# Optimization experiments

Measured on AMD Instinct MI355X. Metric: run time of the kernel, lower is better.

The kernel has to match this reference:

```python
import jax, jax.numpy as jnp
import numpy as np

B, L, H = 2, 2048, 2048
DI, N, DTR, K = 4096, 16, 128, 4  # intermediate, state, dt_rank, conv kernel


def setup_inputs() -> dict:
    key = jax.random.key(0)
    ks = jax.random.split(key, 8)
    x = jax.random.normal(ks[0], (B, L, H), jnp.float32)
    in_proj_w = jax.random.normal(ks[1], (2 * DI, H), jnp.float32) * 0.02
    conv1d_w = jax.random.normal(ks[2], (DI, 1, K), jnp.float32) * 0.1
    conv1d_b = jnp.zeros((DI,), jnp.float32)
    x_proj_w = jax.random.normal(ks[3], (DTR + 2 * N, DI), jnp.float32) * 0.02
    bound = DTR ** -0.5
    dt_proj_w = jax.random.uniform(ks[4], (DI, DTR), jnp.float32, -bound, bound)
    # faithful dt bias init: inverse-softplus of dt ~ Uniform-log[0.001, 0.1]
    dt = jnp.exp(jax.random.uniform(ks[5], (DI,), jnp.float32)
                 * (np.log(0.1) - np.log(0.001)) + np.log(0.001))
    dt = jnp.clip(dt, 1e-4)
    dt_proj_b = dt + jnp.log(-jnp.expm1(-dt))
    A_log = jnp.log(jnp.broadcast_to(jnp.arange(1, N + 1, dtype=jnp.float32), (DI, N)))
    D = jnp.ones((DI,), jnp.float32)
    out_proj_w = jax.random.normal(ks[6], (H, DI), jnp.float32) * 0.02
    return dict(x=x, in_proj_w=in_proj_w, conv1d_w=conv1d_w, conv1d_b=conv1d_b,
                x_proj_w=x_proj_w, dt_proj_w=dt_proj_w, dt_proj_b=dt_proj_b,
                A_log=A_log, D=D, out_proj_w=out_proj_w)


def _mamba_forward(x, in_proj_w, conv1d_w, conv1d_b, x_proj_w,
                   dt_proj_w, dt_proj_b, A_log, D, out_proj_w):
    # in_proj -> split into ssm input and gate (res)
    x_and_res = jnp.einsum('blh,eh->ble', x, in_proj_w)          # [B,L,2*DI]
    xi, res = jnp.split(x_and_res, 2, axis=-1)                    # [B,L,DI] each

    # depthwise causal conv1d (kernel K, left-pad K-1, truncated to L)
    xc = jnp.transpose(xi, (0, 2, 1))                             # [B,DI,L]
    xc = jax.lax.conv_general_dilated(
        xc, conv1d_w, window_strides=(1,), padding=((K - 1, 0),),
        dimension_numbers=('NCH', 'OIH', 'NCH'), feature_group_count=DI)
    xc = xc + conv1d_b[None, :, None]
    u = jax.nn.silu(jnp.transpose(xc, (0, 2, 1)))                 # [B,L,DI]

    # selective SSM parameters
    A = -jnp.exp(A_log.astype(jnp.float32))                       # [DI,N]
    x_dbl = jnp.einsum('bld,ed->ble', u, x_proj_w)                # [B,L,DTR+2N]
    dlt, Bm, Cm = jnp.split(x_dbl, [DTR, DTR + N], axis=-1)
    delta = jax.nn.softplus(jnp.einsum('blr,dr->bld', dlt, dt_proj_w) + dt_proj_b)

    # selective scan over time; carry h: [B,DI,N]
    def step(h, inp):
        d_t, B_t, C_t, u_t = inp                                  # [B,DI],[B,N],[B,N],[B,DI]
        dA = jnp.exp(d_t[:, :, None] * A)                         # [B,DI,N]
        h = dA * h + d_t[:, :, None] * B_t[:, None, :] * u_t[:, :, None]
        y_t = jnp.einsum('bdn,bn->bd', h, C_t)
        return h, y_t

    xs = (jnp.transpose(delta, (1, 0, 2)), jnp.transpose(Bm, (1, 0, 2)),
          jnp.transpose(Cm, (1, 0, 2)), jnp.transpose(u, (1, 0, 2)))
    h0 = jnp.zeros((x.shape[0], DI, N), jnp.float32)
    _, ys = jax.lax.scan(step, h0, xs)                            # ys: [L,B,DI]
    y = jnp.transpose(ys, (1, 0, 2)) + u * D.astype(jnp.float32)  # skip via D

    y = y * jax.nn.silu(res)                                      # gate
    return jnp.einsum('bld,hd->blh', y, out_proj_w)               # [B,L,H]


def reference(x, in_proj_w, conv1d_w, conv1d_b, x_proj_w,
              dt_proj_w, dt_proj_b, A_log, D, out_proj_w):
    return _mamba_forward(x, in_proj_w, conv1d_w, conv1d_b, x_proj_w,
                          dt_proj_w, dt_proj_b, A_log, D, out_proj_w)
```

## Files before the change

kernel.cpp:

```cpp
#include <hip/hip_runtime.h>
#include <hip/hip_bf16.h>
#include <stdint.h>

#define DEV static __device__ __forceinline__

typedef __attribute__((ext_vector_type(8))) short short8;
typedef __attribute__((ext_vector_type(4))) float f32x4;
typedef __attribute__((address_space(3))) void lds_void;
typedef __attribute__((address_space(1))) void glb_void;

constexpr int CB = 2, CL = 2048, CH = 2048, CDI = 4096, CN = 16, CDTR = 128;
constexpr int BLR = CB * CL;
constexpr int NC = 32, LC = 64;
constexpr int KSL = 8;

DEV ushort f2b(float f) {
  union { float f; uint32_t u; } v; v.f = f;
  uint32_t u = v.u;
  return (ushort)((u + 0x7fffu + ((u >> 16) & 1u)) >> 16);
}
DEV float b2f(ushort b) {
  union { uint32_t u; float f; } v; v.u = ((uint32_t)b) << 16;
  return v.f;
}
DEV void gload16(const ushort* g, ushort* l) {
  __builtin_amdgcn_global_load_lds((const glb_void*)g, (lds_void*)l, 16, 0, 0);
}
DEV f32x4 mfma16(short8 a, short8 b, f32x4 c) {
  return __builtin_amdgcn_mfma_f32_16x16x32_bf16(a, b, c, 0, 0, 0);
}

__global__ void cast_kernel(const float* __restrict__ in, ushort* __restrict__ out, int n4) {
  int i = blockIdx.x * blockDim.x + threadIdx.x;
  if (i >= n4) return;
  float4 v = *(const float4*)(in + (size_t)i * 4);
  *(ushort4*)(out + (size_t)i * 4) = make_ushort4(f2b(v.x), f2b(v.y), f2b(v.z), f2b(v.w));
}

__global__ void cast_pad_xproj_kernel(const float* __restrict__ in, ushort* __restrict__ out) {
  int i = blockIdx.x * blockDim.x + threadIdx.x;
  if (i >= (256 * 4096 / 4)) return;
  int idx = i * 4;
  int r = idx >> 12;
  ushort4 o;
  if (r < 160) {
    float4 v = *(const float4*)(in + idx);
    o = make_ushort4(f2b(v.x), f2b(v.y), f2b(v.z), f2b(v.w));
  } else {
    o = make_ushort4(0, 0, 0, 0);
  }
  *(ushort4*)(out + idx) = o;
}

__global__ void conv_silu_kernel(const ushort* __restrict__ xr, const float* __restrict__ w,
                                 const float* __restrict__ bias, ushort* __restrict__ u) {
  int t = blockIdx.x * blockDim.x + threadIdx.x;
  if (t >= BLR * CDI / 8) return;
  const int d8 = (t & (CDI / 8 - 1)) << 3;
  const int bl = t >> 9;
  const int l = bl & (CL - 1);
  float a[8];
  {
    float4 b0 = *(const float4*)(bias + d8);
    float4 b1 = *(const float4*)(bias + d8 + 4);
    a[0] = b0.x; a[1] = b0.y; a[2] = b0.z; a[3] = b0.w;
    a[4] = b1.x; a[5] = b1.y; a[6] = b1.z; a[7] = b1.w;
  }
  float wk[8][4];
#pragma unroll
  for (int j = 0; j < 8; ++j) {
    float4 wj = *(const float4*)(w + (size_t)(d8 + j) * 4);
    wk[j][0] = wj.x; wk[j][1] = wj.y; wk[j][2] = wj.z; wk[j][3] = wj.w;
  }
#pragma unroll
  for (int k = 0; k < 4; ++k) {
    if (l - 3 + k >= 0) {
      short8 xv = *(const short8*)(xr + (size_t)(bl - 3 + k) * 8192 + d8);
#pragma unroll
      for (int j = 0; j < 8; ++j)
        a[j] = fmaf(wk[j][k], b2f((ushort)xv[j]), a[j]);
    }
  }
  short8 o;
#pragma unroll
  for (int j = 0; j < 8; ++j) {
    float s = a[j] / (1.f + __expf(-a[j]));
    o[j] = (short)f2b(s);
  }
  *(short8*)(u + (size_t)bl * 4096 + d8) = o;
}

template<int EPI>
__global__ __launch_bounds__(256, 4)
void gemm_bt_kernel(const ushort* __restrict__ A, const ushort* __restrict__ Bw,
                    void* __restrict__ Cp, const float* __restrict__ bias,
                    int M, int N, int K) {
  __shared__ ushort sA[128 * 32];
  __shared__ ushort sB[128 * 32];
  const int tid = threadIdx.x;
  const int bm = blockIdx.x, bn = blockIdx.y;
  const int w = tid >> 6, l = tid & 63;
  const int wr = w >> 1, wc = w & 1;
  const int q = l >> 4, r = l & 15;

  f32x4 acc[4][4] = {};

  const ushort* Ab = A + (size_t)bm * 128 * K;
  const ushort* Bb = Bw + (size_t)bn * 128 * K;
  const int nk = K >> 5;
  for (int kt = 0; kt < nk; ++kt) {
    const int k0 = kt << 5;
#pragma unroll
    for (int i = 0; i < 2; ++i) {
      const int chunk = i * 256 + tid;
      const int row = chunk >> 2;
      const int cofs = (chunk & 3) << 3;
      gload16(Ab + (size_t)row * K + k0 + cofs, sA + chunk * 8);
      gload16(Bb + (size_t)row * K + k0 + cofs, sB + chunk * 8);
    }
    __syncthreads();
    short8 af[4], bfg[4];
#pragma unroll
    for (int i = 0; i < 4; ++i) {
      af[i]  = *(const short8*)(sA + (wr * 64 + i * 16 + r) * 32 + q * 8);
      bfg[i] = *(const short8*)(sB + (wc * 64 + i * 16 + r) * 32 + q * 8);
    }
#pragma unroll
    for (int i = 0; i < 4; ++i)
#pragma unroll
      for (int j = 0; j < 4; ++j)
        acc[i][j] = mfma16(af[i], bfg[j], acc[i][j]);
    __syncthreads();
  }

  const int m0 = bm * 128 + wr * 64;
  const int n0 = bn * 128 + wc * 64;
#pragma unroll
  for (int i = 0; i < 4; ++i) {
#pragma unroll
    for (int j = 0; j < 4; ++j) {
#pragma unroll
      for (int v = 0; v < 4; ++v) {
        const int grow = m0 + i * 16 + q * 4 + v;
        const int gcol = n0 + j * 16 + r;
        const float val = acc[i][j][v];
        if (EPI == 0) {
          ((ushort*)Cp)[(size_t)grow * N + gcol] = f2b(val);
        } else if (EPI == 1) {
          ((float*)Cp)[(size_t)grow * N + gcol] = val;
        } else {
          float xv = val + bias[gcol];
          float sp = xv > 20.f ? xv : log1pf(__expf(xv));
          ((ushort*)Cp)[(size_t)grow * N + gcol] = f2b(sp);
        }
      }
    }
  }
}

template<int EPI>
__global__ __launch_bounds__(512, 1)
void gemm256p_kernel(const ushort* __restrict__ A, const ushort* __restrict__ Bw,
                     void* __restrict__ Cp, int N, int K) {
  __shared__ ushort sA[2][16384];
  __shared__ ushort sB[2][16384];
  const int tid = threadIdx.x;
  const int bm = blockIdx.x, bn = blockIdx.y;
  const int wid = tid >> 6, l = tid & 63;
  const int wr = wid >> 2, wc = wid & 3;
  const int q = l >> 4, r = l & 15;
  const int rx = r & 7;
  const int nt = K >> 6;

  const ushort* Ab = A + (size_t)bm * 256 * K;
  const ushort* Bb = Bw + (size_t)bn * 256 * K;

  const int srow = tid >> 3;
  const int sxor = (tid & 7) ^ (srow & 7);

  auto stageA = [&](int T, int j) {
    const int Ts = (T < nt) ? T : (nt - 1);
    gload16(Ab + (size_t)(j * 64 + srow) * K + Ts * 64 + sxor * 8,
            &sA[T & 1][0] + j * 4096 + tid * 8);
  };
  auto stageB = [&](int T, int j) {
    const int Ts = (T < nt) ? T : (nt - 1);
    gload16(Bb + (size_t)(j * 64 + srow) * K + Ts * 64 + sxor * 8,
            &sB[T & 1][0] + j * 4096 + tid * 8);
  };

  const int sl0 = (q ^ rx) * 8;
  const int sl1 = ((4 + q) ^ rx) * 8;

  f32x4 acc[8][4] = {};

  stageA(0, 1); stageA(0, 3);
  stageB(0, 0); stageA(0, 0);
  stageB(0, 2); stageA(0, 2);
  stageB(0, 1); stageB(0, 3);
  stageA(1, 1); stageA(1, 3);
  asm volatile("s_waitcnt vmcnt(2)" ::: "memory");
  __builtin_amdgcn_s_barrier();

#define PHASE(M0, M1, S0, S1, LAST)                                        \
  {                                                                        \
    const int ra0 = (wr * 128 + (M0) * 16 + r) * 64;                       \
    const int ra1 = (wr * 128 + (M1) * 16 + r) * 64;                       \
    short8 a00 = *(const short8*)(At + ra0 + sl0);                         \
    short8 a01 = *(const short8*)(At + ra0 + sl1);                         \
    short8 a10 = *(const short8*)(At + ra1 + sl0);                         \
    short8 a11 = *(const short8*)(At + ra1 + sl1);                         \
    S0; S1;                                                                \
    if (LAST) asm volatile("s_waitcnt vmcnt(2)" ::: "memory");             \
    __builtin_amdgcn_s_barrier();                                          \
    asm volatile("s_waitcnt lgkmcnt(0)" ::: "memory");                     \
    __builtin_amdgcn_sched_barrier(0);                                     \
    __builtin_amdgcn_s_setprio(1);                                         \
    _Pragma("unroll")                                                      \
    for (int n = 0; n < 4; ++n) {                                          \
      acc[M0][n] = mfma16(a00, bf[n][0], acc[M0][n]);                      \
      acc[M0][n] = mfma16(a01, bf[n][1], acc[M0][n]);                      \
      acc[M1][n] = mfma16(a10, bf[n][0], acc[M1][n]);                      \
      acc[M1][n] = mfma16(a11, bf[n][1], acc[M1][n]);                      \
    }                                                                      \
    __builtin_amdgcn_s_setprio(0);                                         \
    __builtin_amdgcn_sched_barrier(0);                                     \
    __builtin_amdgcn_s_barrier();                                          \
  }

  for (int t = 0; t < nt; ++t) {
    const ushort* At = &sA[t & 1][0];
    const ushort* Bt = &sB[t & 1][0];
    short8 bf[4][2];
#pragma unroll
    for (int n = 0; n < 4; ++n) {
      const int br = (wc * 64 + n * 16 + r) * 64;
      bf[n][0] = *(const short8*)(Bt + br + sl0);
      bf[n][1] = *(const short8*)(Bt + br + sl1);
    }
    PHASE(6, 7, stageB(t + 1, 0), stageA(t + 1, 0), false)
    PHASE(4, 5, stageB(t + 1, 2), stageA(t + 1, 2), false)
    PHASE(2, 3, stageB(t + 1, 1), stageB(t + 1, 3), false)
    PHASE(0, 1, stageA(t + 2, 1), stageA(t + 2, 3), true)
  }
#undef PHASE

  const int m0g = bm * 256 + wr * 128;
  const int n0g = bn * 256 + wc * 64;
#pragma unroll
  for (int m = 0; m < 8; ++m)
#pragma unroll
    for (int n = 0; n < 4; ++n)
#pragma unroll
      for (int v = 0; v < 4; ++v) {
        const int grow = m0g + m * 16 + q * 4 + v;
        const int gcol = n0g + n * 16 + r;
        if (EPI == 0) ((ushort*)Cp)[(size_t)grow * N + gcol] = f2b(acc[m][n][v]);
        else          ((float*)Cp)[(size_t)grow * N + gcol]  = acc[m][n][v];
      }
}

template<int EPI>
__global__ __launch_bounds__(512, 1)
void gemm128x256_kernel(const ushort* __restrict__ A, const ushort* __restrict__ Bw,
                        void* __restrict__ Cp, int N, int K) {
  __shared__ ushort sA[3][8192];
  __shared__ ushort sB[3][16384];
  const int tid = threadIdx.x;
  const int bm = blockIdx.x, bn = blockIdx.y;
  const int wid = tid >> 6, l = tid & 63;
  const int wr = wid >> 2, wc = wid & 3;
  const int q = l >> 4, r = l & 15;
  const int rx = r & 7;
  const int nt = K >> 6;

  const ushort* Ab = A + (size_t)bm * 128 * K;
  const ushort* Bb = Bw + (size_t)bn * 256 * K;

  const int srow = tid >> 3;
  const int sxor = (tid & 7) ^ (srow & 7);

  auto stageA = [&](int T, int buf, int j) {
    const int Ts = (T < nt) ? T : (nt - 1);
    gload16(Ab + (size_t)(j * 64 + srow) * K + Ts * 64 + sxor * 8,
            &sA[buf][0] + j * 4096 + tid * 8);
  };
  auto stageB = [&](int T, int buf, int j) {
    const int Ts = (T < nt) ? T : (nt - 1);
    gload16(Bb + (size_t)(j * 64 + srow) * K + Ts * 64 + sxor * 8,
            &sB[buf][0] + j * 4096 + tid * 8);
  };

  const int sl0 = (q ^ rx) * 8;
  const int sl1 = ((4 + q) ^ rx) * 8;

  f32x4 acc[4][4] = {};

  stageA(0, 0, 0); stageA(0, 0, 1);
  stageB(0, 0, 0); stageB(0, 0, 1); stageB(0, 0, 2); stageB(0, 0, 3);
  stageA(1, 1, 0); stageA(1, 1, 1);
  asm volatile("s_waitcnt vmcnt(2)" ::: "memory");
  __builtin_amdgcn_s_barrier();

  int c0 = 0;
  for (int t = 0; t < nt; ++t) {
    const int c1 = (c0 == 2) ? 0 : c0 + 1;
    const int c2 = (c1 == 2) ? 0 : c1 + 1;
    const ushort* At = &sA[c0][0];
    const ushort* Bt = &sB[c0][0];
    short8 bf[4][2];
#pragma unroll
    for (int n = 0; n < 4; ++n) {
      const int br = (wc * 64 + n * 16 + r) * 64;
      bf[n][0] = *(const short8*)(Bt + br + sl0);
      bf[n][1] = *(const short8*)(Bt + br + sl1);
    }
    {
      const int ra0 = (wr * 64 + 2 * 16 + r) * 64;
      const int ra1 = (wr * 64 + 3 * 16 + r) * 64;
      short8 a00 = *(const short8*)(At + ra0 + sl0);
      short8 a01 = *(const short8*)(At + ra0 + sl1);
      short8 a10 = *(const short8*)(At + ra1 + sl0);
      short8 a11 = *(const short8*)(At + ra1 + sl1);
      stageB(t + 1, c1, 0); stageB(t + 1, c1, 1); stageB(t + 1, c1, 2);
      __builtin_amdgcn_s_barrier();
      asm volatile("s_waitcnt lgkmcnt(0)" ::: "memory");
      __builtin_amdgcn_sched_barrier(0);
      __builtin_amdgcn_s_setprio(1);
#pragma unroll
      for (int n = 0; n < 4; ++n) {
        acc[2][n] = mfma16(a00, bf[n][0], acc[2][n]);
        acc[2][n] = mfma16(a01, bf[n][1], acc[2][n]);
        acc[3][n] = mfma16(a10, bf[n][0], acc[3][n]);
        acc[3][n] = mfma16(a11, bf[n][1], acc[3][n]);
      }
      __builtin_amdgcn_s_setprio(0);
      __builtin_amdgcn_sched_barrier(0);
      __builtin_amdgcn_s_barrier();
    }
    {
      const int ra0 = (wr * 64 + 0 * 16 + r) * 64;
      const int ra1 = (wr * 64 + 1 * 16 + r) * 64;
      short8 a00 = *(const short8*)(At + ra0 + sl0);
      short8 a01 = *(const short8*)(At + ra0 + sl1);
      short8 a10 = *(const short8*)(At + ra1 + sl0);
      short8 a11 = *(const short8*)(At + ra1 + sl1);
      stageB(t + 1, c1, 3); stageA(t + 2, c2, 0); stageA(t + 2, c2, 1);
      asm volatile("s_waitcnt vmcnt(2)" ::: "memory");
      __builtin_amdgcn_s_barrier();
      asm volatile("s_waitcnt lgkmcnt(0)" ::: "memory");
      __builtin_amdgcn_sched_barrier(0);
      __builtin_amdgcn_s_setprio(1);
#pragma unroll
      for (int n = 0; n < 4; ++n) {
        acc[0][n] = mfma16(a00, bf[n][0], acc[0][n]);
        acc[0][n] = mfma16(a01, bf[n][1], acc[0][n]);
        acc[1][n] = mfma16(a10, bf[n][0], acc[1][n]);
        acc[1][n] = mfma16(a11, bf[n][1], acc[1][n]);
      }
      __builtin_amdgcn_s_setprio(0);
      __builtin_amdgcn_sched_barrier(0);
      __builtin_amdgcn_s_barrier();
    }
    c0 = c1;
  }

  const int m0g = bm * 128 + wr * 64;
  const int n0g = bn * 256 + wc * 64;
#pragma unroll
  for (int m = 0; m < 4; ++m)
#pragma unroll
    for (int n = 0; n < 4; ++n)
#pragma unroll
      for (int v = 0; v < 4; ++v) {
        const int grow = m0g + m * 16 + q * 4 + v;
        const int gcol = n0g + n * 16 + r;
        if (EPI == 0) ((ushort*)Cp)[(size_t)grow * N + gcol] = f2b(acc[m][n][v]);
        else          ((float*)Cp)[(size_t)grow * N + gcol]  = acc[m][n][v];
      }
}

__global__ __launch_bounds__(512, 1)
void gemm3_kernel(const ushort* __restrict__ A, const ushort* __restrict__ Bw,
                  ushort* __restrict__ Cp, const float* __restrict__ bias) {
  __shared__ ushort sA[256 * 128];
  __shared__ ushort sB[256 * 128];
  const int tid = threadIdx.x;
  const int bm = blockIdx.x, bn = blockIdx.y;
  const int wid = tid >> 6, l = tid & 63;
  const int wr = wid >> 2, wc = wid & 3;
  const int q = l >> 4, r = l & 15;

  const ushort* Ab = A + (size_t)bm * 256 * 128;
  const ushort* Bb = Bw + (size_t)bn * 256 * 128;
#pragma unroll
  for (int i = 0; i < 8; ++i) {
    const int c = i * 512 + tid;
    const int row = c >> 4, p = c & 15;
    const int lsl = p ^ (row & 7);
    gload16(Ab + (size_t)row * 128 + lsl * 8, sA + c * 8);
    gload16(Bb + (size_t)row * 128 + lsl * 8, sB + c * 8);
  }
  __syncthreads();

  f32x4 acc[8][4] = {};
  short8 bf[4][4];
#pragma unroll
  for (int n = 0; n < 4; ++n) {
    const int brow = wc * 64 + n * 16 + r;
#pragma unroll
    for (int ks = 0; ks < 4; ++ks) {
      const int p = (ks * 4 + q) ^ (brow & 7);
      bf[n][ks] = *(const short8*)(sB + brow * 128 + p * 8);
    }
  }
#pragma unroll
  for (int m = 0; m < 8; ++m) {
    const int arow = wr * 128 + m * 16 + r;
    short8 af[4];
#pragma unroll
    for (int ks = 0; ks < 4; ++ks) {
      const int p = (ks * 4 + q) ^ (arow & 7);
      af[ks] = *(const short8*)(sA + arow * 128 + p * 8);
    }
#pragma unroll
    for (int ks = 0; ks < 4; ++ks)
#pragma unroll
      for (int n = 0; n < 4; ++n)
        acc[m][n] = mfma16(af[ks], bf[n][ks], acc[m][n]);
  }

  const int m0g = bm * 256 + wr * 128;
  const int n0g = bn * 256 + wc * 64;
#pragma unroll
  for (int m = 0; m < 8; ++m)
#pragma unroll
    for (int n = 0; n < 4; ++n)
#pragma unroll
      for (int v = 0; v < 4; ++v) {
        const int grow = m0g + m * 16 + q * 4 + v;
        const int gcol = n0g + n * 16 + r;
        float xv = acc[m][n][v] + bias[gcol];
        float sp = xv > 20.f ? xv : log1pf(__expf(xv));
        Cp[(size_t)grow * 4096 + gcol] = f2b(sp);
      }
}

__global__ __launch_bounds__(256, 4)
void gemm_btk_kernel(const ushort* __restrict__ A, const ushort* __restrict__ Bw,
                     float* __restrict__ Cpart, int N, int Ktot, int Ksl) {
  __shared__ ushort sA[128 * 32];
  __shared__ ushort sB[128 * 32];
  const int tid = threadIdx.x;
  const int bm = blockIdx.x, bn = blockIdx.y, z = blockIdx.z;
  const int w = tid >> 6, l = tid & 63;
  const int wr = w >> 1, wc = w & 1;
  const int q = l >> 4, r = l & 15;

  f32x4 acc[4][4] = {};

  const ushort* Ab = A + (size_t)bm * 128 * Ktot + z * Ksl;
  const ushort* Bb = Bw + (size_t)bn * 128 * Ktot + z * Ksl;
  const int nk = Ksl >> 5;
  for (int kt = 0; kt < nk; ++kt) {
    const int k0 = kt << 5;
#pragma unroll
    for (int i = 0; i < 2; ++i) {
      const int chunk = i * 256 + tid;
      const int row = chunk >> 2;
      const int cofs = (chunk & 3) << 3;
      gload16(Ab + (size_t)row * Ktot + k0 + cofs, sA + chunk * 8);
      gload16(Bb + (size_t)row * Ktot + k0 + cofs, sB + chunk * 8);
    }
    __syncthreads();
    short8 af[4], bfg[4];
#pragma unroll
    for (int i = 0; i < 4; ++i) {
      af[i]  = *(const short8*)(sA + (wr * 64 + i * 16 + r) * 32 + q * 8);
      bfg[i] = *(const short8*)(sB + (wc * 64 + i * 16 + r) * 32 + q * 8);
    }
#pragma unroll
    for (int i = 0; i < 4; ++i)
#pragma unroll
      for (int j = 0; j < 4; ++j)
        acc[i][j] = mfma16(af[i], bfg[j], acc[i][j]);
    __syncthreads();
  }

  float* Cz = Cpart + (size_t)z * BLR * N;
  const int m0 = bm * 128 + wr * 64;
  const int n0 = bn * 128 + wc * 64;
#pragma unroll
  for (int i = 0; i < 4; ++i)
#pragma unroll
    for (int j = 0; j < 4; ++j)
#pragma unroll
      for (int v = 0; v < 4; ++v)
        Cz[(size_t)(m0 + i * 16 + q * 4 + v) * N + (n0 + j * 16 + r)] = acc[i][j][v];
}

__global__ __launch_bounds__(256)
void reduce_xdbl_kernel(const float* __restrict__ part, float* __restrict__ xdbl,
                        ushort* __restrict__ dlt) {
  const int i = blockIdx.x * 256 + threadIdx.x;
  const int idx = i * 4;
  const int row = idx >> 8, col = idx & 255;
  float4 s = make_float4(0.f, 0.f, 0.f, 0.f);
#pragma unroll
  for (int z = 0; z < KSL; ++z) {
    float4 v = *(const float4*)(part + (size_t)z * BLR * 256 + idx);
    s.x += v.x; s.y += v.y; s.z += v.z; s.w += v.w;
  }
  *(float4*)(xdbl + idx) = s;
  if (col < 128) {
    *(ushort4*)(dlt + (size_t)row * 128 + col) =
        make_ushort4(f2b(s.x), f2b(s.y), f2b(s.z), f2b(s.w));
  }
}

__global__ __launch_bounds__(256)
void scan_pass1_kernel(const ushort* __restrict__ delta_bf, const ushort* __restrict__ u_bf,
                       const float* __restrict__ xdbl, const float* __restrict__ A_log,
                       float* __restrict__ Hc, float* __restrict__ Ssum) {
  __shared__ float4 sB[LC * 4];
  const int blk = blockIdx.x;
  const int dblk = blk & 15, bc = blk >> 4;
  const int b = bc & (CB - 1), c = bc >> 1;
  const int tid = threadIdx.x;
  const int d = dblk * 256 + tid;
  const size_t rowbase = (size_t)b * CL + c * LC;

  {
    const int rr = tid >> 2, seg = tid & 3;
    sB[tid] = *(const float4*)(xdbl + (rowbase + rr) * 256 + 128 + seg * 4);
  }
  __syncthreads();

  float Ae[16];
#pragma unroll
  for (int n = 0; n < 16; ++n) Ae[n] = -__expf(A_log[(size_t)d * CN + n]);
  float h[16] = {};
  float S = 0.f;
  for (int t = 0; t < LC; ++t) {
    const float dl = b2f(delta_bf[(rowbase + t) * 4096 + d]);
    const float uu = b2f(u_bf[(rowbase + t) * 4096 + d]);
    const float du = dl * uu;
    S += dl;
#pragma unroll
    for (int q = 0; q < 4; ++q) {
      float4 bq = sB[t * 4 + q];
      h[q * 4 + 0] = __expf(Ae[q * 4 + 0] * dl) * h[q * 4 + 0] + du * bq.x;
      h[q * 4 + 1] = __expf(Ae[q * 4 + 1] * dl) * h[q * 4 + 1] + du * bq.y;
      h[q * 4 + 2] = __expf(Ae[q * 4 + 2] * dl) * h[q * 4 + 2] + du * bq.z;
      h[q * 4 + 3] = __expf(Ae[q * 4 + 3] * dl) * h[q * 4 + 3] + du * bq.w;
    }
  }
  float4* Hp = (float4*)(Hc + ((((size_t)c * CB + b) * CDI + d) << 4));
#pragma unroll
  for (int q = 0; q < 4; ++q)
    Hp[q] = make_float4(h[q * 4 + 0], h[q * 4 + 1], h[q * 4 + 2], h[q * 4 + 3]);
  Ssum[((size_t)c * CB + b) * CDI + d] = S;
}

__global__ __launch_bounds__(256)
void scan_pass2_kernel(float* __restrict__ Hc, const float* __restrict__ Ssum,
                       const float* __restrict__ A_log) {
  const int t = blockIdx.x * 256 + threadIdx.x;
  const int n = t & 15, d = (t >> 4) & (CDI - 1), b = t >> 16;
  const float Ae = -__expf(A_log[(size_t)d * CN + n]);
  float h = 0.f;
  for (int c = 1; c < NC; ++c) {
    const size_t idxp = ((size_t)(c - 1) * CB + b) * CDI + d;
    const float P = __expf(Ae * Ssum[idxp]);
    h = P * h + Hc[idxp * 16 + n];
    Hc[idxp * 16 + n] = h;
  }
}

__global__ __launch_bounds__(256)
void scan_pass3_kernel(const ushort* __restrict__ delta_bf, const ushort* __restrict__ u_bf,
                       const float* __restrict__ xdbl, const ushort* __restrict__ xr,
                       const float* __restrict__ A_log, const float* __restrict__ Dvec,
                       const float* __restrict__ Hc, ushort* __restrict__ ybf) {
  __shared__ float4 sB[LC * 4];
  __shared__ float4 sC[LC * 4];
  const int blk = blockIdx.x;
  const int dblk = blk & 15, bc = blk >> 4;
  const int b = bc & (CB - 1), c = bc >> 1;
  const int tid = threadIdx.x;
  const int d = dblk * 256 + tid;
  const size_t rowbase = (size_t)b * CL + c * LC;

  {
    const int rr = tid >> 2, seg = tid & 3;
    sB[tid] = *(const float4*)(xdbl + (rowbase + rr) * 256 + 128 + seg * 4);
    sC[tid] = *(const float4*)(xdbl + (rowbase + rr) * 256 + 144 + seg * 4);
  }
  __syncthreads();

  float Ae[16];
#pragma unroll
  for (int n = 0; n < 16; ++n) Ae[n] = -__expf(A_log[(size_t)d * CN + n]);
  float h[16];
  if (c == 0) {
#pragma unroll
    for (int n = 0; n < 16; ++n) h[n] = 0.f;
  } else {
    const float4* Hp = (const float4*)(Hc + ((((size_t)(c - 1) * CB + b) * CDI + d) << 4));
#pragma unroll
    for (int q = 0; q < 4; ++q) {
      float4 hv = Hp[q];
      h[q * 4 + 0] = hv.x; h[q * 4 + 1] = hv.y; h[q * 4 + 2] = hv.z; h[q * 4 + 3] = hv.w;
    }
  }
  const float Dd = Dvec[d];
  for (int t = 0; t < LC; ++t) {
    const float dl = b2f(delta_bf[(rowbase + t) * 4096 + d]);
    const float uu = b2f(u_bf[(rowbase + t) * 4096 + d]);
    const float du = dl * uu;
    float y = 0.f;
#pragma unroll
    for (int q = 0; q < 4; ++q) {
      float4 bq = sB[t * 4 + q];
      float4 cq = sC[t * 4 + q];
      h[q * 4 + 0] = __expf(Ae[q * 4 + 0] * dl) * h[q * 4 + 0] + du * bq.x;
      h[q * 4 + 1] = __expf(Ae[q * 4 + 1] * dl) * h[q * 4 + 1] + du * bq.y;
      h[q * 4 + 2] = __expf(Ae[q * 4 + 2] * dl) * h[q * 4 + 2] + du * bq.z;
      h[q * 4 + 3] = __expf(Ae[q * 4 + 3] * dl) * h[q * 4 + 3] + du * bq.w;
      y = fmaf(h[q * 4 + 0], cq.x, y);
      y = fmaf(h[q * 4 + 1], cq.y, y);
      y = fmaf(h[q * 4 + 2], cq.z, y);
      y = fmaf(h[q * 4 + 3], cq.w, y);
    }
    const float res = b2f(xr[(rowbase + t) * 8192 + 4096 + d]);
    const float sres = res / (1.f + __expf(-res));
    ybf[(rowbase + t) * 4096 + d] = f2b((y + uu * Dd) * sres);
  }
}

extern "C" void kernel_launch(void* const* d_in, const int* in_sizes, int n_in,
                              void* d_out, int out_size, void* d_ws, size_t ws_size,
                              hipStream_t stream) {
  (void)in_sizes; (void)n_in; (void)out_size; (void)ws_size;
  const float* x       = (const float*)d_in[0];
  const float* in_w    = (const float*)d_in[1];
  const float* conv_w  = (const float*)d_in[2];
  const float* conv_b  = (const float*)d_in[3];
  const float* xproj_w = (const float*)d_in[4];
  const float* dt_w    = (const float*)d_in[5];
  const float* dt_b    = (const float*)d_in[6];
  const float* A_log   = (const float*)d_in[7];
  const float* Dvec    = (const float*)d_in[8];
  const float* out_w   = (const float*)d_in[9];
  float* out = (float*)d_out;
  char* ws = (char*)d_ws;
  const size_t MB = 1u << 20;

  ushort* xb    = (ushort*)(ws);
  float*  Hc    = (float*)(ws);
  ushort* wout  = (ushort*)(ws);
  ushort* wb1   = (ushort*)(ws + 16 * MB);
  ushort* u_bf  = (ushort*)(ws + 16 * MB);
  ushort* xr    = (ushort*)(ws + 48 * MB);
  float*  part  = (float*)(ws + 112 * MB);
  ushort* delta = (ushort*)(ws + 112 * MB);
  ushort* ybf   = (ushort*)(ws + 144 * MB);
  float*  xdbl  = (float*)(ws + 176 * MB);
  ushort* dlt   = (ushort*)(ws + 180 * MB);
  ushort* wxp   = (ushort*)(ws + 181 * MB);
  ushort* wdt   = (ushort*)(ws + 183 * MB);
  float*  Ssum  = (float*)(ws + 184 * MB);

  auto cast = [&](const float* in, ushort* o, int n) {
    cast_kernel<<<(n / 4 + 255) / 256, 256, 0, stream>>>(in, o, n / 4);
  };

  cast(x, xb, BLR * CH);
  cast(in_w, wb1, 2 * CDI * CH);
  gemm256p_kernel<0><<<dim3(BLR / 256, (2 * CDI) / 256), 512, 0, stream>>>(
      xb, wb1, xr, 2 * CDI, CH);
  conv_silu_kernel<<<(BLR * CDI / 8) / 256, 256, 0, stream>>>(xr, conv_w, conv_b, u_bf);
  cast_pad_xproj_kernel<<<(256 * 4096 / 4) / 256, 256, 0, stream>>>(xproj_w, wxp);
  gemm_btk_kernel<<<dim3(BLR / 128, 2, KSL), 256, 0, stream>>>(
      u_bf, wxp, part, 256, CDI, CDI / KSL);
  reduce_xdbl_kernel<<<(BLR * 256 / 4) / 256, 256, 0, stream>>>(part, xdbl, dlt);
  cast(dt_w, wdt, CDI * CDTR);
  gemm3_kernel<<<dim3(BLR / 256, CDI / 256), 512, 0, stream>>>(dlt, wdt, delta, dt_b);
  scan_pass1_kernel<<<NC * CB * (CDI / 256), 256, 0, stream>>>(
      delta, u_bf, xdbl, A_log, Hc, Ssum);
  scan_pass2_kernel<<<(CB * CDI * CN) / 256, 256, 0, stream>>>(Hc, Ssum, A_log);
  scan_pass3_kernel<<<NC * CB * (CDI / 256), 256, 0, stream>>>(
      delta, u_bf, xdbl, xr, A_log, Dvec, Hc, ybf);
  cast(out_w, wout, CH * CDI);
  gemm128x256_kernel<1><<<dim3(BLR / 128, CH / 256), 512, 0, stream>>>(
      ybf, wout, out, CH, CDI);
}
```

Before: 549.1 us.

## Switch in_proj GEMM to 32x32x16 MFMA and merge weight cast kernels

Rewrites the 256x256 in_proj GEMM inner loop to use 32x32x16 bf16 MFMA tiles instead of 16x16x32. This cuts the number of MFMA issues and LDS fragment reads per k-tile, and the swizzled LDS addressing and epilogue index mapping change to match. It also folds the x, in_proj, dt_proj and padded x_proj casts into one launch to remove kernel launch overhead, and drops the unused gemm_bt kernel. The larger accumulator layout changes register pressure and the store pattern in the epilogue.

```diff
diff --git a/kernel.cpp b/kernel.cpp
--- a/kernel.cpp
+++ b/kernel.cpp
@@ -6,6 +6,7 @@
 
 typedef __attribute__((ext_vector_type(8))) short short8;
 typedef __attribute__((ext_vector_type(4))) float f32x4;
+typedef __attribute__((ext_vector_type(16))) float f32x16;
 typedef __attribute__((address_space(3))) void lds_void;
 typedef __attribute__((address_space(1))) void glb_void;
 
@@ -28,6 +29,39 @@
 }
 DEV f32x4 mfma16(short8 a, short8 b, f32x4 c) {
   return __builtin_amdgcn_mfma_f32_16x16x32_bf16(a, b, c, 0, 0, 0);
+}
+DEV f32x16 mfma32(short8 a, short8 b, f32x16 c) {
+  return __builtin_amdgcn_mfma_f32_32x32x16_bf16(a, b, c, 0, 0, 0);
+}
+
+constexpr int N4_X  = BLR * CH / 4;
+constexpr int N4_W1 = 2 * CDI * CH / 4;
+constexpr int N4_DT = CDI * CDTR / 4;
+constexpr int N4_XP = 256 * 4096 / 4;
+__global__ void cast_all_kernel(const float* __restrict__ x, const float* __restrict__ in_w,
+                                const float* __restrict__ dt_w, const float* __restrict__ xp_w,
+                                ushort* __restrict__ xb, ushort* __restrict__ wb1,
+                                ushort* __restrict__ wdt, ushort* __restrict__ wxp) {
+  int i = blockIdx.x * 256 + threadIdx.x;
+  const float* src; ushort* dst; int idx;
+  if (i < N4_X) { src = x; dst = xb; idx = i; }
+  else if (i < N4_X + N4_W1) { src = in_w; dst = wb1; idx = i - N4_X; }
+  else if (i < N4_X + N4_W1 + N4_DT) { src = dt_w; dst = wdt; idx = i - N4_X - N4_W1; }
+  else {
+    idx = i - (N4_X + N4_W1 + N4_DT);
+    if (idx >= N4_XP) return;
+    int e = idx * 4;
+    int rr = e >> 12;
+    ushort4 o;
+    if (rr < 160) {
+      float4 v = *(const float4*)(xp_w + e);
+      o = make_ushort4(f2b(v.x), f2b(v.y), f2b(v.z), f2b(v.w));
+    } else o = make_ushort4(0, 0, 0, 0);
+    *(ushort4*)(wxp + e) = o;
+    return;
+  }
+  float4 v = *(const float4*)(src + (size_t)idx * 4);
+  *(ushort4*)(dst + (size_t)idx * 4) = make_ushort4(f2b(v.x), f2b(v.y), f2b(v.z), f2b(v.w));
 }
 
 __global__ void cast_kernel(const float* __restrict__ in, ushort* __restrict__ out, int n4) {
@@ -35,21 +69,6 @@
   if (i >= n4) return;
   float4 v = *(const float4*)(in + (size_t)i * 4);
   *(ushort4*)(out + (size_t)i * 4) = make_ushort4(f2b(v.x), f2b(v.y), f2b(v.z), f2b(v.w));
-}
-
-__global__ void cast_pad_xproj_kernel(const float* __restrict__ in, ushort* __restrict__ out) {
-  int i = blockIdx.x * blockDim.x + threadIdx.x;
-  if (i >= (256 * 4096 / 4)) return;
-  int idx = i * 4;
-  int r = idx >> 12;
-  ushort4 o;
-  if (r < 160) {
-    float4 v = *(const float4*)(in + idx);
-    o = make_ushort4(f2b(v.x), f2b(v.y), f2b(v.z), f2b(v.w));
-  } else {
-    o = make_ushort4(0, 0, 0, 0);
-  }
-  *(ushort4*)(out + idx) = o;
 }
 
 __global__ void conv_silu_kernel(const ushort* __restrict__ xr, const float* __restrict__ w,
@@ -91,76 +110,8 @@
 }
 
 template<int EPI>
-__global__ __launch_bounds__(256, 4)
-void gemm_bt_kernel(const ushort* __restrict__ A, const ushort* __restrict__ Bw,
-                    void* __restrict__ Cp, const float* __restrict__ bias,
-                    int M, int N, int K) {
-  __shared__ ushort sA[128 * 32];
-  __shared__ ushort sB[128 * 32];
-  const int tid = threadIdx.x;
-  const int bm = blockIdx.x, bn = blockIdx.y;
-  const int w = tid >> 6, l = tid & 63;
-  const int wr = w >> 1, wc = w & 1;
-  const int q = l >> 4, r = l & 15;
-
-  f32x4 acc[4][4] = {};
-
-  const ushort* Ab = A + (size_t)bm * 128 * K;
-  const ushort* Bb = Bw + (size_t)bn * 128 * K;
-  const int nk = K >> 5;
-  for (int kt = 0; kt < nk; ++kt) {
-    const int k0 = kt << 5;
-#pragma unroll
-    for (int i = 0; i < 2; ++i) {
-      const int chunk = i * 256 + tid;
-      const int row = chunk >> 2;
-      const int cofs = (chunk & 3) << 3;
-      gload16(Ab + (size_t)row * K + k0 + cofs, sA + chunk * 8);
-      gload16(Bb + (size_t)row * K + k0 + cofs, sB + chunk * 8);
-    }
-    __syncthreads();
-    short8 af[4], bfg[4];
-#pragma unroll
-    for (int i = 0; i < 4; ++i) {
-      af[i]  = *(const short8*)(sA + (wr * 64 + i * 16 + r) * 32 + q * 8);
-      bfg[i] = *(const short8*)(sB + (wc * 64 + i * 16 + r) * 32 + q * 8);
-    }
-#pragma unroll
-    for (int i = 0; i < 4; ++i)
-#pragma unroll
-      for (int j = 0; j < 4; ++j)
-        acc[i][j] = mfma16(af[i], bfg[j], acc[i][j]);
-    __syncthreads();
-  }
-
-  const int m0 = bm * 128 + wr * 64;
-  const int n0 = bn * 128 + wc * 64;
-#pragma unroll
-  for (int i = 0; i < 4; ++i) {
-#pragma unroll
-    for (int j = 0; j < 4; ++j) {
-#pragma unroll
-      for (int v = 0; v < 4; ++v) {
-        const int grow = m0 + i * 16 + q * 4 + v;
-        const int gcol = n0 + j * 16 + r;
-        const float val = acc[i][j][v];
-        if (EPI == 0) {
-          ((ushort*)Cp)[(size_t)grow * N + gcol] = f2b(val);
-        } else if (EPI == 1) {
-          ((float*)Cp)[(size_t)grow * N + gcol] = val;
-        } else {
-          float xv = val + bias[gcol];
-          float sp = xv > 20.f ? xv : log1pf(__expf(xv));
-          ((ushort*)Cp)[(size_t)grow * N + gcol] = f2b(sp);
-        }
-      }
-    }
-  }
-}
-
-template<int EPI>
 __global__ __launch_bounds__(512, 1)
-void gemm256p_kernel(const ushort* __restrict__ A, const ushort* __restrict__ Bw,
+void gemm256w_kernel(const ushort* __restrict__ A, const ushort* __restrict__ Bw,
                      void* __restrict__ Cp, int N, int K) {
   __shared__ ushort sA[2][16384];
   __shared__ ushort sB[2][16384];
@@ -168,8 +119,7 @@
   const int bm = blockIdx.x, bn = blockIdx.y;
   const int wid = tid >> 6, l = tid & 63;
   const int wr = wid >> 2, wc = wid & 3;
-  const int q = l >> 4, r = l & 15;
-  const int rx = r & 7;
+  const int r5 = l & 31, q2 = l >> 5;
   const int nt = K >> 6;
 
   const ushort* Ab = A + (size_t)bm * 256 * K;
@@ -189,10 +139,7 @@
             &sB[T & 1][0] + j * 4096 + tid * 8);
   };
 
-  const int sl0 = (q ^ rx) * 8;
-  const int sl1 = ((4 + q) ^ rx) * 8;
-
-  f32x4 acc[8][4] = {};
+  f32x16 acc[4][2] = {};
 
   stageA(0, 1); stageA(0, 3);
   stageB(0, 0); stageA(0, 0);
@@ -202,27 +149,29 @@
   asm volatile("s_waitcnt vmcnt(2)" ::: "memory");
   __builtin_amdgcn_s_barrier();
 
-#define PHASE(M0, M1, S0, S1, LAST)                                        \
+#define PHASE32(M, S0, S1, LAST)                                           \
   {                                                                        \
-    const int ra0 = (wr * 128 + (M0) * 16 + r) * 64;                       \
-    const int ra1 = (wr * 128 + (M1) * 16 + r) * 64;                       \
-    short8 a00 = *(const short8*)(At + ra0 + sl0);                         \
-    short8 a01 = *(const short8*)(At + ra0 + sl1);                         \
-    short8 a10 = *(const short8*)(At + ra1 + sl0);                         \
-    short8 a11 = *(const short8*)(At + ra1 + sl1);                         \
+    const int arow = wr * 128 + (M) * 32 + r5;                             \
+    const int abase = arow * 64;                                           \
+    const int ax = arow & 7;                                               \
+    short8 a0 = *(const short8*)(At + abase + ((0 | q2) ^ ax) * 8);        \
+    short8 a1 = *(const short8*)(At + abase + ((2 | q2) ^ ax) * 8);        \
+    short8 a2 = *(const short8*)(At + abase + ((4 | q2) ^ ax) * 8);        \
+    short8 a3 = *(const short8*)(At + abase + ((6 | q2) ^ ax) * 8);        \
     S0; S1;                                                                \
     if (LAST) asm volatile("s_waitcnt vmcnt(2)" ::: "memory");             \
     __builtin_amdgcn_s_barrier();                                          \
     asm volatile("s_waitcnt lgkmcnt(0)" ::: "memory");                     \
     __builtin_amdgcn_sched_barrier(0);                                     \
     __builtin_amdgcn_s_setprio(1);                                         \
-    _Pragma("unroll")                                                      \
-    for (int n = 0; n < 4; ++n) {                                          \
-      acc[M0][n] = mfma16(a00, bf[n][0], acc[M0][n]);                      \
-      acc[M0][n] = mfma16(a01, bf[n][1], acc[M0][n]);                      \
-      acc[M1][n] = mfma16(a10, bf[n][0], acc[M1][n]);                      \
-      acc[M1][n] = mfma16(a11, bf[n][1], acc[M1][n]);                      \
-    }                                                                      \
+    acc[M][0] = mfma32(a0, bfr[0][0], acc[M][0]);                          \
+    acc[M][1] = mfma32(a0, bfr[1][0], acc[M][1]);                          \
+    acc[M][0] = mfma32(a1, bfr[0][1], acc[M][0]);                          \
+    acc[M][1] = mfma32(a1, bfr[1][1], acc[M][1]);                          \
+    acc[M][0] = mfma32(a2, bfr[0][2], acc[M][0]);                          \
+    acc[M][1] = mfma32(a2, bfr[1][2], acc[M][1]);                          \
+    acc[M][0] = mfma32(a3, bfr[0][3], acc[M][0]);                          \
+    acc[M][1] = mfma32(a3, bfr[1][3], acc[M][1]);                          \
     __builtin_amdgcn_s_setprio(0);                                         \
     __builtin_amdgcn_sched_barrier(0);                                     \
     __builtin_amdgcn_s_barrier();                                          \
@@ -231,30 +180,33 @@
   for (int t = 0; t < nt; ++t) {
     const ushort* At = &sA[t & 1][0];
     const ushort* Bt = &sB[t & 1][0];
-    short8 bf[4][2];
-#pragma unroll
-    for (int n = 0; n < 4; ++n) {
-      const int br = (wc * 64 + n * 16 + r) * 64;
-      bf[n][0] = *(const short8*)(Bt + br + sl0);
-      bf[n][1] = *(const short8*)(Bt + br + sl1);
-    }
-    PHASE(6, 7, stageB(t + 1, 0), stageA(t + 1, 0), false)
-    PHASE(4, 5, stageB(t + 1, 2), stageA(t + 1, 2), false)
-    PHASE(2, 3, stageB(t + 1, 1), stageB(t + 1, 3), false)
-    PHASE(0, 1, stageA(t + 2, 1), stageA(t + 2, 3), true)
-  }
-#undef PHASE
+    short8 bfr[2][4];
+#pragma unroll
+    for (int n = 0; n < 2; ++n) {
+      const int brow = wc * 64 + n * 32 + r5;
+      const int bbase = brow * 64;
+      const int bx = brow & 7;
+#pragma unroll
+      for (int ks = 0; ks < 4; ++ks)
+        bfr[n][ks] = *(const short8*)(Bt + bbase + (((ks << 1) | q2) ^ bx) * 8);
+    }
+    PHASE32(3, stageB(t + 1, 0), stageA(t + 1, 0), false)
+    PHASE32(2, stageB(t + 1, 2), stageA(t + 1, 2), false)
+    PHASE32(1, stageB(t + 1, 1), stageB(t + 1, 3), false)
+    PHASE32(0, stageA(t + 2, 1), stageA(t + 2, 3), true)
+  }
+#undef PHASE32
 
   const int m0g = bm * 256 + wr * 128;
   const int n0g = bn * 256 + wc * 64;
 #pragma unroll
-  for (int m = 0; m < 8; ++m)
-#pragma unroll
-    for (int n = 0; n < 4; ++n)
-#pragma unroll
-      for (int v = 0; v < 4; ++v) {
-        const int grow = m0g + m * 16 + q * 4 + v;
-        const int gcol = n0g + n * 16 + r;
+  for (int m = 0; m < 4; ++m)
+#pragma unroll
+    for (int n = 0; n < 2; ++n)
+#pragma unroll
+      for (int v = 0; v < 16; ++v) {
+        const int grow = m0g + m * 32 + (v & 3) + ((v >> 2) << 3) + (q2 << 2);
+        const int gcol = n0g + n * 32 + r5;
         if (EPI == 0) ((ushort*)Cp)[(size_t)grow * N + gcol] = f2b(acc[m][n][v]);
         else          ((float*)Cp)[(size_t)grow * N + gcol]  = acc[m][n][v];
       }
@@ -671,27 +623,21 @@
   ushort* wdt   = (ushort*)(ws + 183 * MB);
   float*  Ssum  = (float*)(ws + 184 * MB);
 
-  auto cast = [&](const float* in, ushort* o, int n) {
-    cast_kernel<<<(n / 4 + 255) / 256, 256, 0, stream>>>(in, o, n / 4);
-  };
-
-  cast(x, xb, BLR * CH);
-  cast(in_w, wb1, 2 * CDI * CH);
-  gemm256p_kernel<0><<<dim3(BLR / 256, (2 * CDI) / 256), 512, 0, stream>>>(
+  cast_all_kernel<<<(N4_X + N4_W1 + N4_DT + N4_XP) / 256, 256, 0, stream>>>(
+      x, in_w, dt_w, xproj_w, xb, wb1, wdt, wxp);
+  gemm256w_kernel<0><<<dim3(BLR / 256, (2 * CDI) / 256), 512, 0, stream>>>(
       xb, wb1, xr, 2 * CDI, CH);
   conv_silu_kernel<<<(BLR * CDI / 8) / 256, 256, 0, stream>>>(xr, conv_w, conv_b, u_bf);
-  cast_pad_xproj_kernel<<<(256 * 4096 / 4) / 256, 256, 0, stream>>>(xproj_w, wxp);
   gemm_btk_kernel<<<dim3(BLR / 128, 2, KSL), 256, 0, stream>>>(
       u_bf, wxp, part, 256, CDI, CDI / KSL);
   reduce_xdbl_kernel<<<(BLR * 256 / 4) / 256, 256, 0, stream>>>(part, xdbl, dlt);
-  cast(dt_w, wdt, CDI * CDTR);
   gemm3_kernel<<<dim3(BLR / 256, CDI / 256), 512, 0, stream>>>(dlt, wdt, delta, dt_b);
   scan_pass1_kernel<<<NC * CB * (CDI / 256), 256, 0, stream>>>(
       delta, u_bf, xdbl, A_log, Hc, Ssum);
   scan_pass2_kernel<<<(CB * CDI * CN) / 256, 256, 0, stream>>>(Hc, Ssum, A_log);
   scan_pass3_kernel<<<NC * CB * (CDI / 256), 256, 0, stream>>>(
       delta, u_bf, xdbl, xr, A_log, Dvec, Hc, ybf);
-  cast(out_w, wout, CH * CDI);
+  cast_kernel<<<(CH * CDI / 4) / 256, 256, 0, stream>>>(out_w, wout, CH * CDI / 4);
   gemm128x256_kernel<1><<<dim3(BLR / 128, CH / 256), 512, 0, stream>>>(
       ybf, wout, out, CH, CDI);
 }
```

After: 565.0 us. +2.9%, slower.
